# Kernel optimization log

Hardware: AMD Instinct MI355X
Metric: run time of the kernel (lower is better)

Reference implementation:

```python
import jax, jax.numpy as jnp
import numpy as np

N_NODES = 50000
N_EDGES = 25000
N_PAIRS = 800000
D = 96


def setup_inputs() -> dict:
    key = jax.random.key(0)
    ks = jax.random.split(key, 7)
    X = jax.random.normal(ks[0], (N_NODES, D), dtype=jnp.float32)
    X0 = jax.random.normal(ks[1], (N_NODES, D), dtype=jnp.float32)
    W = jax.random.normal(ks[2], (D, D), dtype=jnp.float32) / np.sqrt(D)
    degE = jax.random.uniform(ks[3], (N_EDGES, 1), dtype=jnp.float32, minval=0.1, maxval=1.0)
    degV = jax.random.uniform(ks[4], (N_NODES, 1), dtype=jnp.float32, minval=0.1, maxval=1.0)
    vertex = jax.random.randint(ks[5], (N_PAIRS,), 0, N_NODES, dtype=jnp.int32)
    edges = jax.random.randint(ks[6], (N_PAIRS,), 0, N_EDGES, dtype=jnp.int32)
    return {"X": X, "X0": X0, "W": W, "degE": degE, "degV": degV,
            "vertex": vertex, "edges": edges, "alpha": 0.1, "beta": 0.5}


def reference(X, X0, W, degE, degV, vertex, edges, alpha, beta):
    N = X.shape[0]
    E = degE.shape[0]
    # V -> E hop: gather node features per incidence pair, mean-reduce per hyperedge
    Xve = X[vertex]                                                  # [M, D]
    esum = jax.ops.segment_sum(Xve, edges, num_segments=E)           # [E, D]
    cnt = jax.ops.segment_sum(jnp.ones((edges.shape[0], 1), X.dtype), edges, num_segments=E)
    Xe = esum / jnp.maximum(cnt, 1.0)                                # mean aggregate
    Xe = Xe * degE
    # E -> V hop: gather hyperedge features, sum-reduce per node
    Xev = Xe[edges]                                                  # [M, D]
    Xv = jax.ops.segment_sum(Xev, vertex, num_segments=N)            # [N, D]
    Xv = Xv * degV
    # row L2 normalize (norm is detached in the original)
    rownorm = jnp.linalg.norm(Xv, axis=1, keepdims=True)
    scale = jax.lax.stop_gradient(jnp.where(rownorm > 0, 1.0 / rownorm, 0.0))
    Xn = Xv * scale
    # GCNII-style residual + identity-mapped Linear (bias=False)
    Xi = (1.0 - alpha) * Xn + alpha * X0
    return (1.0 - beta) * Xi + beta * (Xi @ W.T)
```

## Files before the change

kernel.cpp:

```cpp
#include <hip/hip_runtime.h>

#define DD 96
#define DQ 24
#define DC 12

typedef __attribute__((ext_vector_type(8))) unsigned short u16x8;
typedef __attribute__((ext_vector_type(8))) short s16x8;
typedef __attribute__((ext_vector_type(4))) float f32x4;

__device__ __forceinline__ unsigned short f2bf(float f) {
    unsigned int u = __builtin_bit_cast(unsigned int, f);
    u += 0x7FFFu + ((u >> 16) & 1u);
    return (unsigned short)(u >> 16);
}
__device__ __forceinline__ float bf2f(unsigned short h) {
    unsigned int u = ((unsigned int)h) << 16;
    return __builtin_bit_cast(float, u);
}

__global__ void zero_i(int* p, int n) {
    int i = blockIdx.x * blockDim.x + threadIdx.x;
    if (i < n) p[i] = 0;
}

__global__ void hist_k(const int* __restrict__ vtx, const int* __restrict__ edg,
                       int* __restrict__ cntV, int* __restrict__ cntE,
                       ushort2* __restrict__ rank, int M) {
    int m = blockIdx.x * blockDim.x + threadIdx.x;
    if (m >= M) return;
    int v = vtx[m];
    int e = edg[m];
    int rE = atomicAdd(&cntE[e], 1);
    int rV = atomicAdd(&cntV[v], 1);
    ushort2 r;
    r.x = (unsigned short)rE;
    r.y = (unsigned short)rV;
    rank[m] = r;
}

__global__ __launch_bounds__(256) void alloc_k(const int* __restrict__ cntE,
                                               int* __restrict__ offE, int E,
                                               const int* __restrict__ cntV,
                                               int* __restrict__ offV, int N,
                                               int* __restrict__ cursors) {
    int t = blockIdx.x * blockDim.x + threadIdx.x;
    int lane = threadIdx.x & 63;
    int Ea = (E + 255) & ~255;
    bool isE = t < Ea;
    int idx = isE ? t : t - Ea;
    int n = isE ? E : N;
    const int* cnt = isE ? cntE : cntV;
    int* off = isE ? offE : offV;
    int* cur = cursors + (isE ? 0 : 1);
    bool act = idx < n;
    int c = act ? cnt[idx] : 0;
    int sc = c;
    #pragma unroll
    for (int d = 1; d < 64; d <<= 1) {
        int o = __shfl_up(sc, d);
        if (lane >= d) sc += o;
    }
    int total = __shfl(sc, 63);
    int base = 0;
    if (lane == 63) base = atomicAdd(cur, total);
    base = __shfl(base, 63);
    if (act) off[idx] = base + sc - c;
}

__global__ void build_k(const int* __restrict__ vtx, const int* __restrict__ edg,
                        const ushort2* __restrict__ rank,
                        const int* __restrict__ offE, const int* __restrict__ offV,
                        int* __restrict__ vlist, int* __restrict__ elist, int M) {
    int m = blockIdx.x * blockDim.x + threadIdx.x;
    if (m >= M) return;
    int v = vtx[m];
    int e = edg[m];
    ushort2 r = rank[m];
    vlist[offE[e] + r.x] = v;
    elist[offV[v] + r.y] = e;
}

__global__ void convX_k(const float4* __restrict__ X, u16x8* __restrict__ Xb, int n8) {
    int t = blockIdx.x * blockDim.x + threadIdx.x;
    if (t >= n8) return;
    float4 a = X[t * 2];
    float4 b = X[t * 2 + 1];
    u16x8 o;
    o[0] = f2bf(a.x); o[1] = f2bf(a.y); o[2] = f2bf(a.z); o[3] = f2bf(a.w);
    o[4] = f2bf(b.x); o[5] = f2bf(b.y); o[6] = f2bf(b.z); o[7] = f2bf(b.w);
    Xb[t] = o;
}

__global__ __launch_bounds__(256) void gather_ve_w(const u16x8* __restrict__ Xb,
                                                   const int* __restrict__ offE,
                                                   const int* __restrict__ cntE,
                                                   const int* __restrict__ vlist,
                                                   const float* __restrict__ degE,
                                                   u16x8* __restrict__ Xe, int E) {
    int wid = threadIdx.x >> 6;
    int lane = threadIdx.x & 63;
    int e = blockIdx.x * 4 + wid;
    if (e >= E) return;
    int start = offE[e];
    int cnt = cntE[e];
    int end = start + cnt;
    int part = lane / DC;
    int chunk = lane - part * DC;
    float acc[8] = {0.f, 0.f, 0.f, 0.f, 0.f, 0.f, 0.f, 0.f};
    if (lane < 48) {
        for (int i = start + part; i < end; i += 4) {
            int v = vlist[i];
            u16x8 x = Xb[v * DC + chunk];
            #pragma unroll
            for (int j = 0; j < 8; ++j) acc[j] += bf2f(x[j]);
        }
    }
    #pragma unroll
    for (int j = 0; j < 8; ++j) {
        float o = __shfl(acc[j], (lane + 24) & 63);
        if (lane < 24) acc[j] += o;
    }
    #pragma unroll
    for (int j = 0; j < 8; ++j) {
        float o = __shfl(acc[j], (lane + 12) & 63);
        if (lane < 12) acc[j] += o;
    }
    if (lane < DC) {
        float s = degE[e] / fmaxf((float)cnt, 1.0f);
        u16x8 o;
        #pragma unroll
        for (int j = 0; j < 8; ++j) o[j] = f2bf(acc[j] * s);
        Xe[e * DC + chunk] = o;
    }
}

__global__ __launch_bounds__(256) void gather_norm_w(const u16x8* __restrict__ Xe,
                                                     const int* __restrict__ offV,
                                                     const int* __restrict__ cntV,
                                                     const int* __restrict__ elist,
                                                     const float4* __restrict__ X0,
                                                     const float* __restrict__ degV,
                                                     const float* __restrict__ alpha_p,
                                                     u16x8* __restrict__ Xi, int N) {
    int wid = threadIdx.x >> 6;
    int lane = threadIdx.x & 63;
    int r = blockIdx.x * 4 + wid;
    if (r >= N) return;
    int start = offV[r];
    int end = start + cntV[r];
    int part = lane / DC;
    int chunk = lane - part * DC;
    float acc[8] = {0.f, 0.f, 0.f, 0.f, 0.f, 0.f, 0.f, 0.f};
    if (lane < 48) {
        for (int i = start + part; i < end; i += 4) {
            int e = elist[i];
            u16x8 x = Xe[e * DC + chunk];
            #pragma unroll
            for (int j = 0; j < 8; ++j) acc[j] += bf2f(x[j]);
        }
    }
    #pragma unroll
    for (int j = 0; j < 8; ++j) {
        float o = __shfl(acc[j], (lane + 24) & 63);
        if (lane < 24) acc[j] += o;
    }
    #pragma unroll
    for (int j = 0; j < 8; ++j) {
        float o = __shfl(acc[j], (lane + 12) & 63);
        if (lane < 12) acc[j] += o;
    }
    float ss = 0.f;
    if (lane < DC) {
        float dv = degV[r];
        #pragma unroll
        for (int j = 0; j < 8; ++j) { acc[j] *= dv; ss += acc[j] * acc[j]; }
    }
    #pragma unroll
    for (int off = 32; off; off >>= 1) ss += __shfl_xor(ss, off);
    float scale = (ss > 0.f) ? (1.0f / sqrtf(ss)) : 0.f;
    if (lane < DC) {
        float alpha = *alpha_p;
        float oma = 1.0f - alpha;
        float4 a = X0[r * DQ + chunk * 2];
        float4 b = X0[r * DQ + chunk * 2 + 1];
        float x0v[8] = {a.x, a.y, a.z, a.w, b.x, b.y, b.z, b.w};
        u16x8 o;
        #pragma unroll
        for (int j = 0; j < 8; ++j) o[j] = f2bf(oma * scale * acc[j] + alpha * x0v[j]);
        Xi[r * DC + chunk] = o;
    }
}

__global__ __launch_bounds__(256) void gemm_k(const u16x8* __restrict__ Xi,
                                              const float* __restrict__ W,
                                              const float* __restrict__ beta_p,
                                              float* __restrict__ out, int N) {
    __shared__ unsigned short Ml[DD][104];
    float beta = *beta_p;
    for (int i = threadIdx.x; i < DD * DD; i += 256) {
        int c = i / DD;
        int k = i - c * DD;
        float m = beta * W[i];
        if (c == k) m += 1.0f - beta;
        Ml[c][k] = f2bf(m);
    }
    __syncthreads();
    int wid = threadIdx.x >> 6;
    int lane = threadIdx.x & 63;
    int lrow = lane & 15;
    int lk = (lane >> 4) * 8;
    s16x8 Bf[6][3];
    #pragma unroll
    for (int ct = 0; ct < 6; ++ct)
        #pragma unroll
        for (int ks = 0; ks < 3; ++ks)
            Bf[ct][ks] = *(const s16x8*)&Ml[ct * 16 + lrow][ks * 32 + lk];
    int ntile = (N + 15) / 16;
    int tile = blockIdx.x * 4 + wid;
    if (tile >= ntile) return;
    int r0 = tile * 16;
    const s16x8* xr = (const s16x8*)Xi + (size_t)(r0 + lrow) * DC + (lane >> 4);
    f32x4 acc[6] = {};
    #pragma unroll
    for (int ks = 0; ks < 3; ++ks) {
        s16x8 a = xr[ks * 4];
        #pragma unroll
        for (int ct = 0; ct < 6; ++ct)
            acc[ct] = __builtin_amdgcn_mfma_f32_16x16x32_bf16(a, Bf[ct][ks], acc[ct], 0, 0, 0);
    }
    int orow = r0 + (lane >> 4) * 4;
    #pragma unroll
    for (int ct = 0; ct < 6; ++ct)
        #pragma unroll
        for (int rg = 0; rg < 4; ++rg)
            out[(size_t)(orow + rg) * DD + ct * 16 + lrow] = acc[ct][rg];
}

extern "C" void kernel_launch(void* const* d_in, const int* in_sizes, int n_in,
                              void* d_out, int out_size, void* d_ws, size_t ws_size,
                              hipStream_t stream) {
    const float* X      = (const float*)d_in[0];
    const float* X0     = (const float*)d_in[1];
    const float* W      = (const float*)d_in[2];
    const float* degE   = (const float*)d_in[3];
    const float* degV   = (const float*)d_in[4];
    const int*   vertex = (const int*)d_in[5];
    const int*   edges  = (const int*)d_in[6];
    const float* alpha  = (const float*)d_in[7];
    const float* beta   = (const float*)d_in[8];

    int N = in_sizes[0] / DD;
    int E = in_sizes[3];
    int M = in_sizes[5];

    u16x8* Xb = (u16x8*)d_ws;
    u16x8* Xe = Xb + (size_t)N * DC;
    u16x8* Xi = Xe + (size_t)E * DC;
    int* ip   = (int*)(Xi + (size_t)N * DC);
    int* cntE    = ip;
    int* cntV    = cntE + E;
    int* cursors = cntV + N;
    int* offE    = cursors + 2;
    int* offV    = offE + E;
    ushort2* rank = (ushort2*)(offV + N);
    int* vlist = (int*)(rank + M);
    int* elist = vlist + M;

    zero_i<<<(E + N + 2 + 255) / 256, 256, 0, stream>>>(cntE, E + N + 2);

    hist_k<<<(M + 255) / 256, 256, 0, stream>>>(vertex, edges, cntV, cntE, rank, M);

    convX_k<<<(N * DC + 255) / 256, 256, 0, stream>>>((const float4*)X, Xb, N * DC);

    int Ea = (E + 255) & ~255;
    alloc_k<<<(Ea + N + 255) / 256, 256, 0, stream>>>(cntE, offE, E, cntV, offV, N,
                                                      cursors);

    build_k<<<(M + 255) / 256, 256, 0, stream>>>(vertex, edges, rank, offE, offV,
                                                 vlist, elist, M);

    gather_ve_w<<<(E + 3) / 4, 256, 0, stream>>>(Xb, offE, cntE, vlist, degE, Xe, E);

    gather_norm_w<<<(N + 3) / 4, 256, 0, stream>>>(Xe, offV, cntV, elist,
                                                   (const float4*)X0, degV, alpha, Xi, N);

    int ntile = (N + 15) / 16;
    gemm_k<<<(ntile + 3) / 4, 256, 0, stream>>>(Xi, W, beta, (float*)d_out, N);
}
```

Measured before the change: 200.3 us.

## Fuse gather-normalize with GEMM, merge histogram and conversion, shrink index lists

Several kernels are fused. The E→V gather, normalisation and residual step now writes Xi into LDS, and each wave runs its MFMA tile from there, so the global Xi round trip and one launch are gone. The histogram and the bf16 conversion of X share one launch, and zeroing uses a memset. Index lists shrink to 16-bit and rank is packed into one u32, with vectorised loads in the hist and build kernels. The risks are lower parallelism in the fused kernel (each wave handles 16 rows one after another, and each block builds the W matrix), and the 16-bit indices, which only work while N and E stay below 65536.

```diff
diff --git a/kernel.cpp b/kernel.cpp
--- a/kernel.cpp
+++ b/kernel.cpp
@@ -18,24 +18,42 @@
     return __builtin_bit_cast(float, u);
 }
 
-__global__ void zero_i(int* p, int n) {
-    int i = blockIdx.x * blockDim.x + threadIdx.x;
-    if (i < n) p[i] = 0;
-}
-
-__global__ void hist_k(const int* __restrict__ vtx, const int* __restrict__ edg,
-                       int* __restrict__ cntV, int* __restrict__ cntE,
-                       ushort2* __restrict__ rank, int M) {
-    int m = blockIdx.x * blockDim.x + threadIdx.x;
-    if (m >= M) return;
-    int v = vtx[m];
-    int e = edg[m];
-    int rE = atomicAdd(&cntE[e], 1);
-    int rV = atomicAdd(&cntV[v], 1);
-    ushort2 r;
-    r.x = (unsigned short)rE;
-    r.y = (unsigned short)rV;
-    rank[m] = r;
+__global__ void hist_conv_k(const int* __restrict__ vtx, const int* __restrict__ edg,
+                            int* __restrict__ cntV, int* __restrict__ cntE,
+                            unsigned int* __restrict__ rank, int M, int HB,
+                            const float4* __restrict__ X, u16x8* __restrict__ Xb,
+                            int n8) {
+    if ((int)blockIdx.x >= HB) {
+        int t = (blockIdx.x - HB) * 256 + threadIdx.x;
+        if (t < n8) {
+            float4 a = X[t * 2];
+            float4 b = X[t * 2 + 1];
+            u16x8 o;
+            o[0] = f2bf(a.x); o[1] = f2bf(a.y); o[2] = f2bf(a.z); o[3] = f2bf(a.w);
+            o[4] = f2bf(b.x); o[5] = f2bf(b.y); o[6] = f2bf(b.z); o[7] = f2bf(b.w);
+            Xb[t] = o;
+        }
+        return;
+    }
+    int t = blockIdx.x * 256 + threadIdx.x;
+    int m0 = t * 2;
+    if (m0 + 1 < M) {
+        int2 v2 = *(const int2*)(vtx + m0);
+        int2 e2 = *(const int2*)(edg + m0);
+        unsigned rE0 = atomicAdd(&cntE[e2.x], 1);
+        unsigned rE1 = atomicAdd(&cntE[e2.y], 1);
+        unsigned rV0 = atomicAdd(&cntV[v2.x], 1);
+        unsigned rV1 = atomicAdd(&cntV[v2.y], 1);
+        uint2 r;
+        r.x = (rE0 & 0xFFFFu) | (rV0 << 16);
+        r.y = (rE1 & 0xFFFFu) | (rV1 << 16);
+        *(uint2*)(rank + m0) = r;
+    } else if (m0 < M) {
+        int v = vtx[m0], e = edg[m0];
+        unsigned rE = atomicAdd(&cntE[e], 1);
+        unsigned rV = atomicAdd(&cntV[v], 1);
+        rank[m0] = (rE & 0xFFFFu) | (rV << 16);
+    }
 }
 
 __global__ __launch_bounds__(256) void alloc_k(const int* __restrict__ cntE,
@@ -68,48 +86,54 @@
 }
 
 __global__ void build_k(const int* __restrict__ vtx, const int* __restrict__ edg,
-                        const ushort2* __restrict__ rank,
+                        const unsigned int* __restrict__ rank,
                         const int* __restrict__ offE, const int* __restrict__ offV,
-                        int* __restrict__ vlist, int* __restrict__ elist, int M) {
-    int m = blockIdx.x * blockDim.x + threadIdx.x;
-    if (m >= M) return;
-    int v = vtx[m];
-    int e = edg[m];
-    ushort2 r = rank[m];
-    vlist[offE[e] + r.x] = v;
-    elist[offV[v] + r.y] = e;
-}
-
-__global__ void convX_k(const float4* __restrict__ X, u16x8* __restrict__ Xb, int n8) {
+                        unsigned short* __restrict__ vlist,
+                        unsigned short* __restrict__ elist, int M) {
     int t = blockIdx.x * blockDim.x + threadIdx.x;
-    if (t >= n8) return;
-    float4 a = X[t * 2];
-    float4 b = X[t * 2 + 1];
-    u16x8 o;
-    o[0] = f2bf(a.x); o[1] = f2bf(a.y); o[2] = f2bf(a.z); o[3] = f2bf(a.w);
-    o[4] = f2bf(b.x); o[5] = f2bf(b.y); o[6] = f2bf(b.z); o[7] = f2bf(b.w);
-    Xb[t] = o;
+    int m0 = t * 4;
+    if (m0 + 3 < M) {
+        int4 v4 = *(const int4*)(vtx + m0);
+        int4 e4 = *(const int4*)(edg + m0);
+        uint4 r4 = *(const uint4*)(rank + m0);
+        int oe0 = offE[e4.x], oe1 = offE[e4.y], oe2 = offE[e4.z], oe3 = offE[e4.w];
+        int ov0 = offV[v4.x], ov1 = offV[v4.y], ov2 = offV[v4.z], ov3 = offV[v4.w];
+        vlist[oe0 + (r4.x & 0xFFFFu)] = (unsigned short)v4.x;
+        vlist[oe1 + (r4.y & 0xFFFFu)] = (unsigned short)v4.y;
+        vlist[oe2 + (r4.z & 0xFFFFu)] = (unsigned short)v4.z;
+        vlist[oe3 + (r4.w & 0xFFFFu)] = (unsigned short)v4.w;
+        elist[ov0 + (r4.x >> 16)] = (unsigned short)e4.x;
+        elist[ov1 + (r4.y >> 16)] = (unsigned short)e4.y;
+        elist[ov2 + (r4.z >> 16)] = (unsigned short)e4.z;
+        elist[ov3 + (r4.w >> 16)] = (unsigned short)e4.w;
+    } else {
+        for (int m = m0; m < M; ++m) {
+            int v = vtx[m], e = edg[m];
+            unsigned r = rank[m];
+            vlist[offE[e] + (r & 0xFFFFu)] = (unsigned short)v;
+            elist[offV[v] + (r >> 16)] = (unsigned short)e;
+        }
+    }
 }
 
 __global__ __launch_bounds__(256) void gather_ve_w(const u16x8* __restrict__ Xb,
                                                    const int* __restrict__ offE,
                                                    const int* __restrict__ cntE,
-                                                   const int* __restrict__ vlist,
+                                                   const unsigned short* __restrict__ vlist,
                                                    const float* __restrict__ degE,
                                                    u16x8* __restrict__ Xe, int E) {
     int wid = threadIdx.x >> 6;
     int lane = threadIdx.x & 63;
     int e = blockIdx.x * 4 + wid;
     if (e >= E) return;
-    int start = offE[e];
     int cnt = cntE[e];
-    int end = start + cnt;
+    const unsigned short* seg = vlist + offE[e];
     int part = lane / DC;
     int chunk = lane - part * DC;
     float acc[8] = {0.f, 0.f, 0.f, 0.f, 0.f, 0.f, 0.f, 0.f};
     if (lane < 48) {
-        for (int i = start + part; i < end; i += 4) {
-            int v = vlist[i];
+        for (int i = part; i < cnt; i += 4) {
+            int v = seg[i];
             u16x8 x = Xb[v * DC + chunk];
             #pragma unroll
             for (int j = 0; j < 8; ++j) acc[j] += bf2f(x[j]);
@@ -134,68 +158,18 @@
     }
 }
 
-__global__ __launch_bounds__(256) void gather_norm_w(const u16x8* __restrict__ Xe,
-                                                     const int* __restrict__ offV,
-                                                     const int* __restrict__ cntV,
-                                                     const int* __restrict__ elist,
-                                                     const float4* __restrict__ X0,
-                                                     const float* __restrict__ degV,
-                                                     const float* __restrict__ alpha_p,
-                                                     u16x8* __restrict__ Xi, int N) {
-    int wid = threadIdx.x >> 6;
-    int lane = threadIdx.x & 63;
-    int r = blockIdx.x * 4 + wid;
-    if (r >= N) return;
-    int start = offV[r];
-    int end = start + cntV[r];
-    int part = lane / DC;
-    int chunk = lane - part * DC;
-    float acc[8] = {0.f, 0.f, 0.f, 0.f, 0.f, 0.f, 0.f, 0.f};
-    if (lane < 48) {
-        for (int i = start + part; i < end; i += 4) {
-            int e = elist[i];
-            u16x8 x = Xe[e * DC + chunk];
-            #pragma unroll
-            for (int j = 0; j < 8; ++j) acc[j] += bf2f(x[j]);
-        }
-    }
-    #pragma unroll
-    for (int j = 0; j < 8; ++j) {
-        float o = __shfl(acc[j], (lane + 24) & 63);
-        if (lane < 24) acc[j] += o;
-    }
-    #pragma unroll
-    for (int j = 0; j < 8; ++j) {
-        float o = __shfl(acc[j], (lane + 12) & 63);
-        if (lane < 12) acc[j] += o;
-    }
-    float ss = 0.f;
-    if (lane < DC) {
-        float dv = degV[r];
-        #pragma unroll
-        for (int j = 0; j < 8; ++j) { acc[j] *= dv; ss += acc[j] * acc[j]; }
-    }
-    #pragma unroll
-    for (int off = 32; off; off >>= 1) ss += __shfl_xor(ss, off);
-    float scale = (ss > 0.f) ? (1.0f / sqrtf(ss)) : 0.f;
-    if (lane < DC) {
-        float alpha = *alpha_p;
-        float oma = 1.0f - alpha;
-        float4 a = X0[r * DQ + chunk * 2];
-        float4 b = X0[r * DQ + chunk * 2 + 1];
-        float x0v[8] = {a.x, a.y, a.z, a.w, b.x, b.y, b.z, b.w};
-        u16x8 o;
-        #pragma unroll
-        for (int j = 0; j < 8; ++j) o[j] = f2bf(oma * scale * acc[j] + alpha * x0v[j]);
-        Xi[r * DC + chunk] = o;
-    }
-}
-
-__global__ __launch_bounds__(256) void gemm_k(const u16x8* __restrict__ Xi,
-                                              const float* __restrict__ W,
-                                              const float* __restrict__ beta_p,
-                                              float* __restrict__ out, int N) {
+__global__ __launch_bounds__(256) void gnorm_gemm_k(const u16x8* __restrict__ Xe,
+                                                    const int* __restrict__ offV,
+                                                    const int* __restrict__ cntV,
+                                                    const unsigned short* __restrict__ elist,
+                                                    const float4* __restrict__ X0,
+                                                    const float* __restrict__ degV,
+                                                    const float* __restrict__ alpha_p,
+                                                    const float* __restrict__ W,
+                                                    const float* __restrict__ beta_p,
+                                                    float* __restrict__ out, int N) {
     __shared__ unsigned short Ml[DD][104];
+    __shared__ unsigned short XiL[4][16][104];
     float beta = *beta_p;
     for (int i = threadIdx.x; i < DD * DD; i += 256) {
         int c = i / DD;
@@ -207,33 +181,86 @@
     __syncthreads();
     int wid = threadIdx.x >> 6;
     int lane = threadIdx.x & 63;
+    int part = lane / DC;
+    int chunk = lane - part * DC;
+    float alpha = *alpha_p;
+    float oma = 1.0f - alpha;
+    int r0 = blockIdx.x * 64 + wid * 16;
+    for (int i = 0; i < 16; ++i) {
+        int r = r0 + i;
+        if (r < N) {
+            int cnt = cntV[r];
+            const unsigned short* seg = elist + offV[r];
+            float acc[8] = {0.f, 0.f, 0.f, 0.f, 0.f, 0.f, 0.f, 0.f};
+            if (lane < 48) {
+                for (int t = part; t < cnt; t += 4) {
+                    int e = seg[t];
+                    u16x8 x = Xe[e * DC + chunk];
+                    #pragma unroll
+                    for (int j = 0; j < 8; ++j) acc[j] += bf2f(x[j]);
+                }
+            }
+            #pragma unroll
+            for (int j = 0; j < 8; ++j) {
+                float o = __shfl(acc[j], (lane + 24) & 63);
+                if (lane < 24) acc[j] += o;
+            }
+            #pragma unroll
+            for (int j = 0; j < 8; ++j) {
+                float o = __shfl(acc[j], (lane + 12) & 63);
+                if (lane < 12) acc[j] += o;
+            }
+            float ss = 0.f;
+            if (lane < DC) {
+                float dv = degV[r];
+                #pragma unroll
+                for (int j = 0; j < 8; ++j) { acc[j] *= dv; ss += acc[j] * acc[j]; }
+            }
+            #pragma unroll
+            for (int off = 32; off; off >>= 1) ss += __shfl_xor(ss, off);
+            float scale = (ss > 0.f) ? (1.0f / sqrtf(ss)) : 0.f;
+            if (lane < DC) {
+                float4 a = X0[r * DQ + chunk * 2];
+                float4 b = X0[r * DQ + chunk * 2 + 1];
+                float x0v[8] = {a.x, a.y, a.z, a.w, b.x, b.y, b.z, b.w};
+                u16x8 o;
+                #pragma unroll
+                for (int j = 0; j < 8; ++j)
+                    o[j] = f2bf(oma * scale * acc[j] + alpha * x0v[j]);
+                *(u16x8*)&XiL[wid][i][chunk * 8] = o;
+            }
+        } else if (lane < DC) {
+            u16x8 z = {};
+            *(u16x8*)&XiL[wid][i][chunk * 8] = z;
+        }
+    }
+    __builtin_amdgcn_wave_barrier();
     int lrow = lane & 15;
-    int lk = (lane >> 4) * 8;
+    int lkq = lane >> 4;
     s16x8 Bf[6][3];
     #pragma unroll
     for (int ct = 0; ct < 6; ++ct)
         #pragma unroll
         for (int ks = 0; ks < 3; ++ks)
-            Bf[ct][ks] = *(const s16x8*)&Ml[ct * 16 + lrow][ks * 32 + lk];
-    int ntile = (N + 15) / 16;
-    int tile = blockIdx.x * 4 + wid;
-    if (tile >= ntile) return;
-    int r0 = tile * 16;
-    const s16x8* xr = (const s16x8*)Xi + (size_t)(r0 + lrow) * DC + (lane >> 4);
-    f32x4 acc[6] = {};
-    #pragma unroll
-    for (int ks = 0; ks < 3; ++ks) {
-        s16x8 a = xr[ks * 4];
+            Bf[ct][ks] = *(const s16x8*)&Ml[ct * 16 + lrow][ks * 32 + lkq * 8];
+    s16x8 af[3];
+    #pragma unroll
+    for (int ks = 0; ks < 3; ++ks)
+        af[ks] = *(const s16x8*)&XiL[wid][lrow][ks * 32 + lkq * 8];
+    f32x4 accd[6] = {};
+    #pragma unroll
+    for (int ks = 0; ks < 3; ++ks)
         #pragma unroll
         for (int ct = 0; ct < 6; ++ct)
-            acc[ct] = __builtin_amdgcn_mfma_f32_16x16x32_bf16(a, Bf[ct][ks], acc[ct], 0, 0, 0);
-    }
-    int orow = r0 + (lane >> 4) * 4;
+            accd[ct] = __builtin_amdgcn_mfma_f32_16x16x32_bf16(af[ks], Bf[ct][ks],
+                                                               accd[ct], 0, 0, 0);
+    int orow = r0 + lkq * 4;
     #pragma unroll
     for (int ct = 0; ct < 6; ++ct)
         #pragma unroll
         for (int rg = 0; rg < 4; ++rg)
-            out[(size_t)(orow + rg) * DD + ct * 16 + lrow] = acc[ct][rg];
+            if (orow + rg < N)
+                out[(size_t)(orow + rg) * DD + ct * 16 + lrow] = accd[ct][rg];
 }
 
 extern "C" void kernel_launch(void* const* d_in, const int* in_sizes, int n_in,
@@ -255,35 +282,33 @@
 
     u16x8* Xb = (u16x8*)d_ws;
     u16x8* Xe = Xb + (size_t)N * DC;
-    u16x8* Xi = Xe + (size_t)E * DC;
-    int* ip   = (int*)(Xi + (size_t)N * DC);
-    int* cntE    = ip;
-    int* cntV    = cntE + E;
+    int* cntE = (int*)(Xe + (size_t)E * DC);
+    int* cntV = cntE + E;
     int* cursors = cntV + N;
-    int* offE    = cursors + 2;
-    int* offV    = offE + E;
-    ushort2* rank = (ushort2*)(offV + N);
-    int* vlist = (int*)(rank + M);
-    int* elist = vlist + M;
-
-    zero_i<<<(E + N + 2 + 255) / 256, 256, 0, stream>>>(cntE, E + N + 2);
-
-    hist_k<<<(M + 255) / 256, 256, 0, stream>>>(vertex, edges, cntV, cntE, rank, M);
-
-    convX_k<<<(N * DC + 255) / 256, 256, 0, stream>>>((const float4*)X, Xb, N * DC);
+    int* offE = cursors + 4;
+    int* offV = offE + E;
+    unsigned int* rank = (unsigned int*)(offV + N);
+    unsigned short* vlist = (unsigned short*)(rank + M);
+    unsigned short* elist = vlist + M;
+
+    hipMemsetAsync(cntE, 0, (size_t)(E + N + 4) * sizeof(int), stream);
+
+    int n8 = N * DC;
+    int HB = ((M + 1) / 2 + 255) / 256;
+    int CB = (n8 + 255) / 256;
+    hist_conv_k<<<HB + CB, 256, 0, stream>>>(vertex, edges, cntV, cntE, rank, M, HB,
+                                             (const float4*)X, Xb, n8);
 
     int Ea = (E + 255) & ~255;
     alloc_k<<<(Ea + N + 255) / 256, 256, 0, stream>>>(cntE, offE, E, cntV, offV, N,
                                                       cursors);
 
-    build_k<<<(M + 255) / 256, 256, 0, stream>>>(vertex, edges, rank, offE, offV,
-                                                 vlist, elist, M);
+    build_k<<<((M + 3) / 4 + 255) / 256, 256, 0, stream>>>(vertex, edges, rank,
+                                                           offE, offV, vlist, elist, M);
 
     gather_ve_w<<<(E + 3) / 4, 256, 0, stream>>>(Xb, offE, cntE, vlist, degE, Xe, E);
 
-    gather_norm_w<<<(N + 3) / 4, 256, 0, stream>>>(Xe, offV, cntV, elist,
-                                                   (const float4*)X0, degV, alpha, Xi, N);
-
-    int ntile = (N + 15) / 16;
-    gemm_k<<<(ntile + 3) / 4, 256, 0, stream>>>(Xi, W, beta, (float*)d_out, N);
-}
+    gnorm_gemm_k<<<(N + 63) / 64, 256, 0, stream>>>(Xe, offV, cntV, elist,
+                                                    (const float4*)X0, degV, alpha,
+                                                    W, beta, (float*)d_out, N);
+}
```

New measurement: 230.6 us. +15.1%, slower.
